# Performance work log

Measured on AMD Instinct MI355X. Metric: run time of the kernel, lower is better.

The kernel has to match this reference:

```python
import jax, jax.numpy as jnp
import numpy as np

B, T, C = 4, 2048, 1024
N_HEAD = 16
HEAD_DIM = C // N_HEAD
SCALE = 1.0 / np.sqrt(HEAD_DIM).astype(np.float32)


def setup_inputs() -> dict:
    key = jax.random.key(0)
    k1, k2, k3 = jax.random.split(key, 3)
    x = jax.random.normal(k1, (B, T, C), dtype=jnp.float32)
    # torch Linear weights: [out_features, in_features], scaled init
    w_qkv = jax.random.normal(k2, (3 * C, C), dtype=jnp.float32) * (1.0 / np.sqrt(C))
    w_out = jax.random.normal(k3, (C, C), dtype=jnp.float32) * (1.0 / np.sqrt(C))
    b_out = jnp.zeros((C,), dtype=jnp.float32)
    return {"x": x, "w_qkv": w_qkv, "w_out": w_out, "b_out": b_out}


def reference(x, w_qkv, w_out, b_out):
    Bsz, Tlen, Cdim = x.shape
    qkv = jnp.einsum('btc,oc->bto', x, w_qkv)  # [B,T,3C]
    q, k, v = jnp.split(qkv, 3, axis=-1)
    # [B,H,T,D]
    def heads(t):
        return t.reshape(Bsz, Tlen, N_HEAD, HEAD_DIM).transpose(0, 2, 1, 3)
    q, k, v = heads(q), heads(k), heads(v)
    att = jnp.einsum('bhqd,bhkd->bhqk', q, k) * SCALE  # [B,H,T,T]
    causal = jnp.tril(jnp.ones((Tlen, Tlen), dtype=bool))
    att = jnp.where(causal[None, None], att, -jnp.inf)
    att = jax.nn.softmax(att, axis=-1)
    out = jnp.einsum('bhqk,bhkd->bhqd', att, v)
    out = out.transpose(0, 2, 1, 3).reshape(Bsz, Tlen, Cdim)
    out = jnp.einsum('btc,oc->bto', out, w_out) + b_out
    return out
```

## Files before the change

### kernel.cpp

```cpp
#include <hip/hip_runtime.h>
#include <stdint.h>


typedef __attribute__((ext_vector_type(8))) short bf16x8;
typedef __attribute__((ext_vector_type(4))) float f32x4;

#define EXP2F(x) __builtin_amdgcn_exp2f(x)
#define SL2E 0.18033688011112042f
#define FIXED_M 15.0f

__device__ __forceinline__ short f2bf(float f) {
  union { float f; unsigned u; } c; c.f = f;
  unsigned u = c.u;
  unsigned r = (u + 0x7fffu + ((u >> 16) & 1u)) >> 16;
  return (short)(unsigned short)r;
}

__device__ __forceinline__ short f2bf_fast(float f) {
  union { float f; unsigned u; } c; c.f = f;
  return (short)(unsigned short)((c.u + 0x8000u) >> 16);
}

__device__ __forceinline__ void llds16(const short* g, short* l) {
  __builtin_amdgcn_global_load_lds(
      (const __attribute__((address_space(1))) unsigned int*)g,
      (__attribute__((address_space(3))) unsigned int*)l, 16, 0, 0);
}

__global__ __launch_bounds__(256) void cast_f32_to_bf16(
    const float* __restrict__ src, short* __restrict__ dst, int n4) {
  int i = blockIdx.x * 256 + threadIdx.x;
  if (i >= n4) return;
  float4 f = ((const float4*)src)[i];
  short4 o;
  o.x = f2bf(f.x); o.y = f2bf(f.y); o.z = f2bf(f.z); o.w = f2bf(f.w);
  ((short4*)dst)[i] = o;
}

__global__ __launch_bounds__(256) void transpose_v(
    const short* __restrict__ V, short* __restrict__ Vt) {
  const int T = 2048;
  __shared__ short lT[64 * 72];
  const int tid = threadIdx.x;
  const int t0 = blockIdx.x * 64;
  const int bh = blockIdx.y;
  const size_t ib = (size_t)bh * T * 64;
  const size_t ob = (size_t)bh * 64 * T;
#pragma unroll
  for (int call = 0; call < 2; ++call) {
    const int c = call * 256 + tid;
    bf16x8 vv = *(const bf16x8*)(V + ib + (size_t)(t0 + (c >> 3)) * 64 + (c & 7) * 8);
#pragma unroll
    for (int jj = 0; jj < 8; ++jj)
      lT[((c & 7) * 8 + jj) * 72 + (c >> 3)] = vv[jj];
  }
  __syncthreads();
#pragma unroll
  for (int call = 0; call < 2; ++call) {
    const int c = call * 256 + tid;
    bf16x8 o = *(const bf16x8*)&lT[(c >> 3) * 72 + (c & 7) * 8];
    *(bf16x8*)(Vt + ob + (size_t)(c >> 3) * T + t0 + (c & 7) * 8) = o;
  }
}

__global__ __launch_bounds__(256) void gemm_qkv(
    const short* __restrict__ A, const short* __restrict__ Bw,
    short* __restrict__ Qo, short* __restrict__ Ko, short* __restrict__ Vo) {
  const int K = 1024;
  __shared__ short lA[128 * 32];
  __shared__ short lB[128 * 32];
  const int tid = threadIdx.x;
  const int lane = tid & 63;
  const int wave = tid >> 6;
  const int m0 = blockIdx.y * 128;
  const int n0 = blockIdx.x * 128;
  const int wm = (wave >> 1) * 64;
  const int wn = (wave & 1) * 64;
  const int mrow = lane & 15;
  const int kq = lane >> 4;

  f32x4 acc[4][4];
#pragma unroll
  for (int i = 0; i < 4; ++i)
#pragma unroll
    for (int j = 0; j < 4; ++j) acc[i][j] = (f32x4){0.f, 0.f, 0.f, 0.f};

  for (int k0 = 0; k0 < K; k0 += 32) {
#pragma unroll
    for (int call = 0; call < 2; ++call) {
      const int cb = call * 256 + wave * 64;
      const int c = cb + lane;
      llds16(A + (size_t)(m0 + (c >> 2)) * K + k0 + (c & 3) * 8, &lA[cb * 8]);
      llds16(Bw + (size_t)(n0 + (c >> 2)) * K + k0 + (c & 3) * 8, &lB[cb * 8]);
    }
    __syncthreads();
    bf16x8 af[4], bfr[4];
#pragma unroll
    for (int i = 0; i < 4; ++i)
      af[i] = *(const bf16x8*)&lA[(wm + i * 16 + mrow) * 32 + kq * 8];
#pragma unroll
    for (int j = 0; j < 4; ++j)
      bfr[j] = *(const bf16x8*)&lB[(wn + j * 16 + mrow) * 32 + kq * 8];
#pragma unroll
    for (int i = 0; i < 4; ++i)
#pragma unroll
      for (int j = 0; j < 4; ++j)
        acc[i][j] = __builtin_amdgcn_mfma_f32_16x16x32_bf16(af[i], bfr[j], acc[i][j], 0, 0, 0);
    __syncthreads();
  }

#pragma unroll
  for (int i = 0; i < 4; ++i) {
    const int m = m0 + wm + i * 16 + kq * 4;
    const int b = m >> 11;
    const int t = m & 2047;
#pragma unroll
    for (int j = 0; j < 4; ++j) {
      const int o = n0 + wn + j * 16 + mrow;
      const int which = o >> 10;
      const int c = o & 1023;
      const int h = c >> 6;
      const int d = c & 63;
      short* dst = which == 0 ? Qo : (which == 1 ? Ko : Vo);
      const float sc_ = (which == 1) ? SL2E : 1.0f;
      const size_t off = ((size_t)(b * 16 + h) * 2048 + t) * 64 + d;
#pragma unroll
      for (int r = 0; r < 4; ++r)
        dst[off + (size_t)r * 64] = f2bf(acc[i][j][r] * sc_);
    }
  }
}

__global__ __launch_bounds__(256) void gemm_out(
    const short* __restrict__ A, const short* __restrict__ Bw,
    const float* __restrict__ bias, float* __restrict__ Out) {
  const int K = 1024;
  __shared__ short lA[128 * 32];
  __shared__ short lB[128 * 32];
  const int tid = threadIdx.x;
  const int lane = tid & 63;
  const int wave = tid >> 6;
  const int m0 = blockIdx.y * 128;
  const int n0 = blockIdx.x * 128;
  const int wm = (wave >> 1) * 64;
  const int wn = (wave & 1) * 64;
  const int mrow = lane & 15;
  const int kq = lane >> 4;

  f32x4 acc[4][4];
#pragma unroll
  for (int i = 0; i < 4; ++i)
#pragma unroll
    for (int j = 0; j < 4; ++j) acc[i][j] = (f32x4){0.f, 0.f, 0.f, 0.f};

  for (int k0 = 0; k0 < K; k0 += 32) {
#pragma unroll
    for (int call = 0; call < 2; ++call) {
      const int cb = call * 256 + wave * 64;
      const int c = cb + lane;
      llds16(A + (size_t)(m0 + (c >> 2)) * K + k0 + (c & 3) * 8, &lA[cb * 8]);
      llds16(Bw + (size_t)(n0 + (c >> 2)) * K + k0 + (c & 3) * 8, &lB[cb * 8]);
    }
    __syncthreads();
    bf16x8 af[4], bfr[4];
#pragma unroll
    for (int i = 0; i < 4; ++i)
      af[i] = *(const bf16x8*)&lA[(wm + i * 16 + mrow) * 32 + kq * 8];
#pragma unroll
    for (int j = 0; j < 4; ++j)
      bfr[j] = *(const bf16x8*)&lB[(wn + j * 16 + mrow) * 32 + kq * 8];
#pragma unroll
    for (int i = 0; i < 4; ++i)
#pragma unroll
      for (int j = 0; j < 4; ++j)
        acc[i][j] = __builtin_amdgcn_mfma_f32_16x16x32_bf16(af[i], bfr[j], acc[i][j], 0, 0, 0);
    __syncthreads();
  }

#pragma unroll
  for (int i = 0; i < 4; ++i) {
    const int m = m0 + wm + i * 16 + kq * 4;
#pragma unroll
    for (int j = 0; j < 4; ++j) {
      const int n = n0 + wn + j * 16 + mrow;
      const float bb = bias[n];
#pragma unroll
      for (int r = 0; r < 4; ++r)
        Out[(size_t)(m + r) * 1024 + n] = acc[i][j][r] + bb;
    }
  }
}

__global__ __launch_bounds__(256) void flash_attn(
    const short* __restrict__ Qg, const short* __restrict__ Kg,
    const short* __restrict__ Vtg, short* __restrict__ Og) {
  const int T = 2048;
  __shared__ short lK[2][64 * 64];
  __shared__ short lVt[2][64 * 64];
  __shared__ short lP[4 * 16 * 76];
  const int tid = threadIdx.x;
  const int lane = tid & 63;
  const int wave = tid >> 6;
  const int bh = blockIdx.y;
  const int mrow = lane & 15;
  const int kq = lane >> 4;
  const int swz = mrow & 7;
  const size_t base = (size_t)bh * T * 64;
  const size_t vbase = (size_t)bh * 64 * T;
  const int qtA = blockIdx.x;
  const int qtB = 31 - qtA;

  bf16x8 aqA0, aqA1, aqB0, aqB1;
  {
    const short* qpA = Qg + base + (size_t)(qtA * 64 + wave * 16 + mrow) * 64 + kq * 8;
    aqA0 = *(const bf16x8*)qpA;
    aqA1 = *(const bf16x8*)(qpA + 32);
    const short* qpB = Qg + base + (size_t)(qtB * 64 + wave * 16 + mrow) * 64 + kq * 8;
    aqB0 = *(const bf16x8*)qpB;
    aqB1 = *(const bf16x8*)(qpB + 32);
  }

  f32x4 accA[4], accB[4];
  float lA4[4], lB4[4];
#pragma unroll
  for (int jd = 0; jd < 4; ++jd) {
    accA[jd] = (f32x4){0.f, 0.f, 0.f, 0.f};
    accB[jd] = (f32x4){0.f, 0.f, 0.f, 0.f};
  }
#pragma unroll
  for (int r = 0; r < 4; ++r) { lA4[r] = 0.f; lB4[r] = 0.f; }

  auto stage = [&](int nt, int buf) {
#pragma unroll
    for (int call = 0; call < 2; ++call) {
      const int cb = call * 256 + wave * 64;
      const int c = cb + lane;
      const int row = c >> 3;
      const int scol = (c & 7) ^ (row & 7);
      llds16(Kg + base + (size_t)(nt * 64 + row) * 64 + scol * 8, &lK[buf][cb * 8]);
      llds16(Vtg + vbase + (size_t)row * T + nt * 64 + scol * 8, &lVt[buf][cb * 8]);
    }
  };

  stage(0, 0);
  __syncthreads();

  for (int kt = 0; kt <= qtB; ++kt) {
    const int bcur = kt & 1;
    if (kt < qtB) stage(kt + 1, bcur ^ 1);
    const short* K_ = lK[bcur];
    const short* Vt_ = lVt[bcur];

    auto seg_compute = [&](int qt, bf16x8 aq0, bf16x8 aq1, f32x4* acc, float* l4) {
      f32x4 sc[4];
#pragma unroll
      for (int j = 0; j < 4; ++j) {
        const short* krow = &K_[(j * 16 + mrow) * 64];
        bf16x8 kb0 = *(const bf16x8*)&krow[(kq ^ swz) * 8];
        bf16x8 kb1 = *(const bf16x8*)&krow[((4 + kq) ^ swz) * 8];
        f32x4 s = (f32x4){-FIXED_M, -FIXED_M, -FIXED_M, -FIXED_M};
        s = __builtin_amdgcn_mfma_f32_16x16x32_bf16(aq0, kb0, s, 0, 0, 0);
        s = __builtin_amdgcn_mfma_f32_16x16x32_bf16(aq1, kb1, s, 0, 0, 0);
        sc[j] = s;
      }

      if (kt == qt) {
        const int qrow = qt * 64 + wave * 16 + kq * 4;
#pragma unroll
        for (int j = 0; j < 4; ++j) {
          const int key = kt * 64 + j * 16 + mrow;
#pragma unroll
          for (int r = 0; r < 4; ++r)
            if (key > qrow + r) sc[j][r] = -1e30f;
        }
      }

      short* pw = &lP[wave * 1216];
#pragma unroll
      for (int j = 0; j < 4; ++j)
#pragma unroll
        for (int r = 0; r < 4; ++r) {
          const float p = EXP2F(sc[j][r]);
          l4[r] += p;
          pw[(kq * 4 + r) * 76 + j * 16 + mrow] = f2bf_fast(p);
        }

      bf16x8 pa0 = *(const bf16x8*)&lP[wave * 1216 + mrow * 76 + kq * 8];
      bf16x8 pa1 = *(const bf16x8*)&lP[wave * 1216 + mrow * 76 + 32 + kq * 8];
#pragma unroll
      for (int jd = 0; jd < 4; ++jd) {
        const short* vrow = &Vt_[(jd * 16 + mrow) * 64];
        bf16x8 vb0 = *(const bf16x8*)&vrow[(kq ^ swz) * 8];
        bf16x8 vb1 = *(const bf16x8*)&vrow[((4 + kq) ^ swz) * 8];
        acc[jd] = __builtin_amdgcn_mfma_f32_16x16x32_bf16(pa0, vb0, acc[jd], 0, 0, 0);
        acc[jd] = __builtin_amdgcn_mfma_f32_16x16x32_bf16(pa1, vb1, acc[jd], 0, 0, 0);
      }
    };

    if (kt <= qtA) seg_compute(qtA, aqA0, aqA1, accA, lA4);
    seg_compute(qtB, aqB0, aqB1, accB, lB4);
    __syncthreads();
  }

  const int b = bh >> 4;
  const int h = bh & 15;
#pragma unroll
  for (int off = 1; off < 16; off <<= 1)
#pragma unroll
    for (int r = 0; r < 4; ++r) {
      lA4[r] += __shfl_xor(lA4[r], off);
      lB4[r] += __shfl_xor(lB4[r], off);
    }
#pragma unroll
  for (int r = 0; r < 4; ++r) {
    const float invA = 1.0f / lA4[r];
    const float invB = 1.0f / lB4[r];
    const int tA = qtA * 64 + wave * 16 + kq * 4 + r;
    const int tB = qtB * 64 + wave * 16 + kq * 4 + r;
#pragma unroll
    for (int jd = 0; jd < 4; ++jd) {
      const int col = h * 64 + jd * 16 + mrow;
      Og[((size_t)b * 2048 + tA) * 1024 + col] = f2bf(accA[jd][r] * invA);
      Og[((size_t)b * 2048 + tB) * 1024 + col] = f2bf(accB[jd][r] * invB);
    }
  }
}

extern "C" void kernel_launch(void* const* d_in, const int* in_sizes, int n_in,
                              void* d_out, int out_size, void* d_ws, size_t ws_size,
                              hipStream_t stream) {
  const float* x = (const float*)d_in[0];
  const float* w_qkv = (const float*)d_in[1];
  const float* w_out = (const float*)d_in[2];
  const float* b_out = (const float*)d_in[3];
  float* out = (float*)d_out;

  char* ws = (char*)d_ws;
  const size_t NX = 8192ull * 1024;
  const size_t NWQ = 3072ull * 1024;
  const size_t NWO = 1024ull * 1024;
  const size_t NQ = 64ull * 2048 * 64;
  size_t off = 0;
  short* xb    = (short*)(ws + off); off += NX * 2;
  short* wqkvb = (short*)(ws + off); off += NWQ * 2;
  short* woutb = (short*)(ws + off); off += NWO * 2;
  short* q     = (short*)(ws + off); off += NQ * 2;
  short* k     = (short*)(ws + off); off += NQ * 2;
  short* v     = (short*)(ws + off); off += NQ * 2;
  short* attb  = (short*)(ws + off); off += NX * 2;
  short* vt    = xb;
  if (off > ws_size) return;

  cast_f32_to_bf16<<<(int)(NX / 4 / 256), 256, 0, stream>>>(x, xb, (int)(NX / 4));
  cast_f32_to_bf16<<<(int)(NWQ / 4 / 256), 256, 0, stream>>>(w_qkv, wqkvb, (int)(NWQ / 4));
  cast_f32_to_bf16<<<(int)(NWO / 4 / 256), 256, 0, stream>>>(w_out, woutb, (int)(NWO / 4));
  gemm_qkv<<<dim3(24, 64), 256, 0, stream>>>(xb, wqkvb, q, k, v);
  transpose_v<<<dim3(32, 64), 256, 0, stream>>>(v, vt);
  flash_attn<<<dim3(16, 64), 256, 0, stream>>>(q, k, vt, attb);
  gemm_out<<<dim3(8, 64), 256, 0, stream>>>(attb, woutb, b_out, out);
}
```

Before: 279.3 us.

## Stage QKV epilogue through LDS, compute softmax row sums via MFMA, reorder attention grid

The QKV GEMM epilogue now writes the tile into an LDS buffer and then does coalesced 16-byte stores into Q/K/V, replacing scattered 2-byte stores. In flash attention, the per-lane exp accumulation and the cross-lane shuffle reduction for row sums are replaced by an extra MFMA against a ones vector, so the row sums match the bf16 P actually used. P is converted to bf16 by truncation instead of rounding. The attention grid is swapped so consecutive blocks span heads rather than query tiles. The extra 33KB of LDS in the GEMM may reduce occupancy.

Result: faster. 270.5 us (-3.2%).

```diff
diff --git a/kernel.cpp b/kernel.cpp
--- a/kernel.cpp
+++ b/kernel.cpp
@@ -16,9 +16,9 @@
   return (short)(unsigned short)r;
 }
 
-__device__ __forceinline__ short f2bf_fast(float f) {
+__device__ __forceinline__ short f2bf_trunc(float f) {
   union { float f; unsigned u; } c; c.f = f;
-  return (short)(unsigned short)((c.u + 0x8000u) >> 16);
+  return (short)(unsigned short)(c.u >> 16);
 }
 
 __device__ __forceinline__ void llds16(const short* g, short* l) {
@@ -69,6 +69,7 @@
   const int K = 1024;
   __shared__ short lA[128 * 32];
   __shared__ short lB[128 * 32];
+  __shared__ short lC[128 * 132];
   const int tid = threadIdx.x;
   const int lane = tid & 63;
   const int wave = tid >> 6;
@@ -111,23 +112,33 @@
 
 #pragma unroll
   for (int i = 0; i < 4; ++i) {
-    const int m = m0 + wm + i * 16 + kq * 4;
+    const int row = wm + i * 16 + kq * 4;
+#pragma unroll
+    for (int j = 0; j < 4; ++j) {
+      const int col = wn + j * 16 + mrow;
+      const float sc_ = (((n0 + col) >> 10) == 1) ? SL2E : 1.0f;
+#pragma unroll
+      for (int r = 0; r < 4; ++r)
+        lC[(row + r) * 132 + col] = f2bf(acc[i][j][r] * sc_);
+    }
+  }
+  __syncthreads();
+
+#pragma unroll
+  for (int call = 0; call < 8; ++call) {
+    const int cc = call * 256 + tid;
+    const int row = cc >> 4;
+    const int m = m0 + row;
     const int b = m >> 11;
     const int t = m & 2047;
-#pragma unroll
-    for (int j = 0; j < 4; ++j) {
-      const int o = n0 + wn + j * 16 + mrow;
-      const int which = o >> 10;
-      const int c = o & 1023;
-      const int h = c >> 6;
-      const int d = c & 63;
-      short* dst = which == 0 ? Qo : (which == 1 ? Ko : Vo);
-      const float sc_ = (which == 1) ? SL2E : 1.0f;
-      const size_t off = ((size_t)(b * 16 + h) * 2048 + t) * 64 + d;
-#pragma unroll
-      for (int r = 0; r < 4; ++r)
-        dst[off + (size_t)r * 64] = f2bf(acc[i][j][r] * sc_);
-    }
+    const int o = n0 + (cc & 15) * 8;
+    const int which = o >> 10;
+    const int c = o & 1023;
+    const int h = c >> 6;
+    const int d = c & 63;
+    short* dst = which == 0 ? Qo : (which == 1 ? Ko : Vo);
+    bf16x8 val = *(const bf16x8*)&lC[row * 132 + (cc & 15) * 8];
+    *(bf16x8*)(dst + ((size_t)(b * 16 + h) * 2048 + t) * 64 + d) = val;
   }
 }
 
@@ -201,14 +212,16 @@
   const int tid = threadIdx.x;
   const int lane = tid & 63;
   const int wave = tid >> 6;
-  const int bh = blockIdx.y;
+  const int bh = blockIdx.x;
   const int mrow = lane & 15;
   const int kq = lane >> 4;
   const int swz = mrow & 7;
   const size_t base = (size_t)bh * T * 64;
   const size_t vbase = (size_t)bh * 64 * T;
-  const int qtA = blockIdx.x;
+  const int qtA = blockIdx.y;
   const int qtB = 31 - qtA;
+
+  const bf16x8 ones = {0x3F80, 0x3F80, 0x3F80, 0x3F80, 0x3F80, 0x3F80, 0x3F80, 0x3F80};
 
   bf16x8 aqA0, aqA1, aqB0, aqB1;
   {
@@ -220,15 +233,14 @@
     aqB1 = *(const bf16x8*)(qpB + 32);
   }
 
-  f32x4 accA[4], accB[4];
-  float lA4[4], lB4[4];
+  f32x4 accA[4], accB[4], lacA, lacB;
 #pragma unroll
   for (int jd = 0; jd < 4; ++jd) {
     accA[jd] = (f32x4){0.f, 0.f, 0.f, 0.f};
     accB[jd] = (f32x4){0.f, 0.f, 0.f, 0.f};
   }
-#pragma unroll
-  for (int r = 0; r < 4; ++r) { lA4[r] = 0.f; lB4[r] = 0.f; }
+  lacA = (f32x4){0.f, 0.f, 0.f, 0.f};
+  lacB = (f32x4){0.f, 0.f, 0.f, 0.f};
 
   auto stage = [&](int nt, int buf) {
 #pragma unroll
@@ -251,7 +263,7 @@
     const short* K_ = lK[bcur];
     const short* Vt_ = lVt[bcur];
 
-    auto seg_compute = [&](int qt, bf16x8 aq0, bf16x8 aq1, f32x4* acc, float* l4) {
+    auto seg_compute = [&](int qt, bf16x8 aq0, bf16x8 aq1, f32x4* acc, f32x4& lac) {
       f32x4 sc[4];
 #pragma unroll
       for (int j = 0; j < 4; ++j) {
@@ -279,14 +291,13 @@
 #pragma unroll
       for (int j = 0; j < 4; ++j)
 #pragma unroll
-        for (int r = 0; r < 4; ++r) {
-          const float p = EXP2F(sc[j][r]);
-          l4[r] += p;
-          pw[(kq * 4 + r) * 76 + j * 16 + mrow] = f2bf_fast(p);
-        }
+        for (int r = 0; r < 4; ++r)
+          pw[(kq * 4 + r) * 76 + j * 16 + mrow] = f2bf_trunc(EXP2F(sc[j][r]));
 
       bf16x8 pa0 = *(const bf16x8*)&lP[wave * 1216 + mrow * 76 + kq * 8];
       bf16x8 pa1 = *(const bf16x8*)&lP[wave * 1216 + mrow * 76 + 32 + kq * 8];
+      lac = __builtin_amdgcn_mfma_f32_16x16x32_bf16(pa0, ones, lac, 0, 0, 0);
+      lac = __builtin_amdgcn_mfma_f32_16x16x32_bf16(pa1, ones, lac, 0, 0, 0);
 #pragma unroll
       for (int jd = 0; jd < 4; ++jd) {
         const short* vrow = &Vt_[(jd * 16 + mrow) * 64];
@@ -297,24 +308,17 @@
       }
     };
 
-    if (kt <= qtA) seg_compute(qtA, aqA0, aqA1, accA, lA4);
-    seg_compute(qtB, aqB0, aqB1, accB, lB4);
+    if (kt <= qtA) seg_compute(qtA, aqA0, aqA1, accA, lacA);
+    seg_compute(qtB, aqB0, aqB1, accB, lacB);
     __syncthreads();
   }
 
   const int b = bh >> 4;
   const int h = bh & 15;
 #pragma unroll
-  for (int off = 1; off < 16; off <<= 1)
-#pragma unroll
-    for (int r = 0; r < 4; ++r) {
-      lA4[r] += __shfl_xor(lA4[r], off);
-      lB4[r] += __shfl_xor(lB4[r], off);
-    }
-#pragma unroll
   for (int r = 0; r < 4; ++r) {
-    const float invA = 1.0f / lA4[r];
-    const float invB = 1.0f / lB4[r];
+    const float invA = 1.0f / lacA[r];
+    const float invB = 1.0f / lacB[r];
     const int tA = qtA * 64 + wave * 16 + kq * 4 + r;
     const int tB = qtB * 64 + wave * 16 + kq * 4 + r;
 #pragma unroll
@@ -356,6 +360,6 @@
   cast_f32_to_bf16<<<(int)(NWO / 4 / 256), 256, 0, stream>>>(w_out, woutb, (int)(NWO / 4));
   gemm_qkv<<<dim3(24, 64), 256, 0, stream>>>(xb, wqkvb, q, k, v);
   transpose_v<<<dim3(32, 64), 256, 0, stream>>>(v, vt);
-  flash_attn<<<dim3(16, 64), 256, 0, stream>>>(q, k, vt, attb);
+  flash_attn<<<dim3(64, 16), 256, 0, stream>>>(q, k, vt, attb);
   gemm_out<<<dim3(8, 64), 256, 0, stream>>>(attb, woutb, b_out, out);
 }
```
